# Kernel optimization log

Hardware: AMD Instinct MI355X
Metric: run time of the kernel (lower is better)

The kernel has to match this reference:

```python
import jax, jax.numpy as jnp
import numpy as np

B, H, D = 16, 16, 128          # batch (decode seqs), heads, head_dim
BLK = 16                        # paged-KV block size (hard-coded in source)
MAXB = 128                      # blocks per sequence
MAXS = MAXB * BLK               # 2048 max context
NBLK = B * MAXB                 # total cache blocks
SOFTMAX_SCALE = 1.0 / np.sqrt(D)


def setup_inputs() -> dict:
    key = jax.random.key(0)
    ks = jax.random.split(key, 8)
    Q = jax.random.normal(ks[0], (B, H, D), dtype=jnp.float32)
    K = jax.random.normal(ks[1], (B, H, D), dtype=jnp.float32)
    V = jax.random.normal(ks[2], (B, H, D), dtype=jnp.float32)
    Kcache = jax.random.normal(ks[3], (NBLK, BLK, H, D), dtype=jnp.float32)
    Vcache = jax.random.normal(ks[4], (NBLK, BLK, H, D), dtype=jnp.float32)
    # context length per sequence (includes the new decode token)
    input_length = jax.random.randint(ks[5], (B,), 1, MAXS + 1).astype(jnp.int32)
    # each sequence owns a contiguous run of blocks
    block_tables = jnp.arange(B * MAXB, dtype=jnp.int32).reshape(B, MAXB)
    # flat slot index where the new token's K/V are written
    pos = input_length - 1
    save_slots = (block_tables[jnp.arange(B), pos // BLK] * BLK + pos % BLK).astype(jnp.int64)
    # per-token RoPE cos/sin
    ang = jax.random.uniform(ks[6], (B, D), dtype=jnp.float32) * (2.0 * np.pi)
    cos, sin = jnp.cos(ang), jnp.sin(ang)
    mask = jnp.zeros((B, MAXS), dtype=jnp.float32)  # additive attention bias
    return {"Q": Q, "K": K, "V": V, "Kcache": Kcache, "Vcache": Vcache,
            "cos": cos, "sin": sin, "mask": mask,
            "input_length": input_length, "save_slots": save_slots,
            "block_tables": block_tables, "max_s": MAXS}


def _rope(x, cos, sin):
    # LLaMA rotate-half RoPE; cos/sin are [B,1,D], x is [B,H,D]
    d2 = x.shape[-1] // 2
    x1, x2 = x[..., :d2], x[..., d2:]
    rot = jnp.concatenate([-x2, x1], axis=-1)
    return x * cos + rot * sin


def reference(Q, K, V, Kcache, Vcache, cos, sin, mask,
              input_length, save_slots, block_tables, max_s):
    c = cos[:, None, :]
    s = sin[:, None, :]
    qr = _rope(Q, c, s)                      # [B,H,D]
    kr = _rope(K, c, s)                      # [B,H,D]
    # scatter new token K/V into the paged cache (flat slot view)
    Kf = Kcache.reshape(-1, H, D).at[save_slots].set(kr)
    Vf = Vcache.reshape(-1, H, D).at[save_slots].set(V)
    # gather each sequence's context slots via its block table
    slot_idx = (block_tables[:, :, None] * BLK
                + jnp.arange(BLK, dtype=jnp.int32)).reshape(B, MAXS)  # [B,S]
    keys = Kf[slot_idx]                      # [B,S,H,D]
    vals = Vf[slot_idx]                      # [B,S,H,D]
    scores = jnp.einsum('bhd,bshd->bhs', qr, keys) * SOFTMAX_SCALE + mask[:, None, :]
    valid = jnp.arange(MAXS, dtype=jnp.int32)[None, :] < input_length[:, None]
    scores = jnp.where(valid[:, None, :], scores, jnp.float32(-1e30))
    p = jax.nn.softmax(scores, axis=-1)
    out = jnp.einsum('bhs,bshd->bhd', p, vals)  # [B,H,D]
    return out
```

## Files before the change

kernel.cpp:

```cpp
#include <hip/hip_runtime.h>
#include <hip/hip_bf16.h>

#define BATCH 16
#define NHEAD 16
#define DHEAD 128
#define BLK   16
#define MAXB  128
#define MAXS  (MAXB * BLK)
#define NSPLIT 8
#define CHUNK  (MAXS / NSPLIT)
#define SCALE  0.0883883476483184f

#define WSQ_FLOATS (BATCH * NHEAD * DHEAD)
#define PART_STRIDE (DHEAD + 2)

__global__ void rope_scatter(const float* __restrict__ Q,
                             const float* __restrict__ K,
                             const float* __restrict__ V,
                             float* __restrict__ Kcache,
                             float* __restrict__ Vcache,
                             const float* __restrict__ cosb,
                             const float* __restrict__ sinb,
                             const int* __restrict__ save_slots,
                             float* __restrict__ ws_q) {
    const int bh = blockIdx.x;
    const int b  = bh / NHEAD;
    const int h  = bh % NHEAD;
    const int d  = threadIdx.x;

    const float c = cosb[b * DHEAD + d];
    const float s = sinb[b * DHEAD + d];

    const size_t qidx = (size_t)bh * DHEAD + d;
    const float qv = Q[qidx];
    const float qrot = (d < DHEAD / 2) ? -Q[qidx + DHEAD / 2] : Q[qidx - DHEAD / 2];
    ws_q[qidx] = qv * c + qrot * s;

    const float kv = K[qidx];
    const float krot = (d < DHEAD / 2) ? -K[qidx + DHEAD / 2] : K[qidx - DHEAD / 2];
    const float kr = kv * c + krot * s;

    const int slot = save_slots[b];
    const size_t cidx = (size_t)slot * (NHEAD * DHEAD) + (size_t)h * DHEAD + d;
    Kcache[cidx] = kr;
    Vcache[cidx] = V[qidx];
}

__global__ __launch_bounds__(256) void attn_partial(
        const float* __restrict__ Kcache,
        const float* __restrict__ Vcache,
        const float* __restrict__ mask,
        const int* __restrict__ input_length,
        const int* __restrict__ block_tables,
        const float* __restrict__ ws_q,
        float* __restrict__ ws_part) {
    const int split = blockIdx.x;
    const int h     = blockIdx.y;
    const int b     = blockIdx.z;
    const int tid   = threadIdx.x;
    const int wave  = tid >> 6;
    const int lane  = tid & 63;

    float* part = ws_part + ((size_t)((b * NHEAD + h) * NSPLIT + split)) * PART_STRIDE;

    const int L  = input_length[b];
    const int s0 = split * CHUNK;
    if (s0 >= L) {
        if (tid < DHEAD) part[tid] = 0.0f;
        if (tid == 0) { part[DHEAD] = -1e30f; part[DHEAD + 1] = 0.0f; }
        return;
    }
    const int n = min(CHUNK, L - s0);

    const float2 q = ((const float2*)(ws_q + (size_t)(b * NHEAD + h) * DHEAD))[lane];

    float m = -1e30f, l = 0.0f;
    float2 acc = make_float2(0.0f, 0.0f);

    for (int i = wave; i < n; i += 4) {
        const int s = s0 + i;
        const int slot = block_tables[b * MAXB + (s >> 4)] * BLK + (s & (BLK - 1));
        const size_t base = (size_t)slot * (NHEAD * DHEAD) + (size_t)h * DHEAD;
        const float2 k = ((const float2*)(Kcache + base))[lane];
        const float2 v = ((const float2*)(Vcache + base))[lane];

        float dot = k.x * q.x + k.y * q.y;
        #pragma unroll
        for (int off = 32; off >= 1; off >>= 1)
            dot += __shfl_xor(dot, off, 64);

        const float score = dot * SCALE + mask[(size_t)b * MAXS + s];
        const float mn    = fmaxf(m, score);
        const float p     = __expf(score - mn);
        const float alpha = __expf(m - mn);
        l = l * alpha + p;
        acc.x = acc.x * alpha + p * v.x;
        acc.y = acc.y * alpha + p * v.y;
        m = mn;
    }

    __shared__ float sm[4], sl[4];
    __shared__ float sacc[4][DHEAD];
    sacc[wave][2 * lane]     = acc.x;
    sacc[wave][2 * lane + 1] = acc.y;
    if (lane == 0) { sm[wave] = m; sl[wave] = l; }
    __syncthreads();

    if (tid < DHEAD) {
        float M = fmaxf(fmaxf(sm[0], sm[1]), fmaxf(sm[2], sm[3]));
        float a = 0.0f;
        #pragma unroll
        for (int w = 0; w < 4; ++w) a += sacc[w][tid] * __expf(sm[w] - M);
        part[tid] = a;
        if (tid == 0) {
            float lt = 0.0f;
            #pragma unroll
            for (int w = 0; w < 4; ++w) lt += sl[w] * __expf(sm[w] - M);
            part[DHEAD] = M;
            part[DHEAD + 1] = lt;
        }
    }
}

__global__ void attn_combine(const float* __restrict__ ws_part,
                             float* __restrict__ out) {
    const int bh = blockIdx.x;
    const int d  = threadIdx.x;

    const float* base = ws_part + (size_t)bh * NSPLIT * PART_STRIDE;

    float M = -1e30f;
    #pragma unroll
    for (int s = 0; s < NSPLIT; ++s)
        M = fmaxf(M, base[s * PART_STRIDE + DHEAD]);

    float lsum = 0.0f, a = 0.0f;
    #pragma unroll
    for (int s = 0; s < NSPLIT; ++s) {
        const float f = __expf(base[s * PART_STRIDE + DHEAD] - M);
        lsum += base[s * PART_STRIDE + DHEAD + 1] * f;
        a    += base[s * PART_STRIDE + d] * f;
    }
    out[(size_t)bh * DHEAD + d] = a / lsum;
}

extern "C" void kernel_launch(void* const* d_in, const int* in_sizes, int n_in,
                              void* d_out, int out_size, void* d_ws, size_t ws_size,
                              hipStream_t stream) {
    const float* Q       = (const float*)d_in[0];
    const float* K       = (const float*)d_in[1];
    const float* V       = (const float*)d_in[2];
    float*       Kcache  = (float*)d_in[3];
    float*       Vcache  = (float*)d_in[4];
    const float* cosb    = (const float*)d_in[5];
    const float* sinb    = (const float*)d_in[6];
    const float* mask    = (const float*)d_in[7];
    const int*   in_len  = (const int*)d_in[8];
    const int*   slots   = (const int*)d_in[9];
    const int*   btab    = (const int*)d_in[10];

    float* ws_q    = (float*)d_ws;
    float* ws_part = ws_q + WSQ_FLOATS;
    float* out     = (float*)d_out;

    rope_scatter<<<BATCH * NHEAD, DHEAD, 0, stream>>>(
        Q, K, V, Kcache, Vcache, cosb, sinb, slots, ws_q);

    dim3 grid2(NSPLIT, NHEAD, BATCH);
    attn_partial<<<grid2, 256, 0, stream>>>(
        Kcache, Vcache, mask, in_len, btab, ws_q, ws_part);

    attn_combine<<<BATCH * NHEAD, DHEAD, 0, stream>>>(ws_part, out);
}
```

Measured before the change: 515.2 us.

## Process tokens with half-wave float4 loads and two tokens per iteration

Each 32-lane half-wave now handles one token using float4 loads of K and V, giving 8 concurrent token streams per block instead of 4. The main loop unrolls by two tokens to issue more independent loads before the shuffle reduction and softmax update. The aim is more memory-level parallelism and fewer shuffle steps in this bandwidth-bound paged attention. The cost is more registers per thread and a larger cross-group merge in shared memory.

New measurement: 492.6 us. -4.4%, faster.

```diff
diff --git a/kernel.cpp b/kernel.cpp
--- a/kernel.cpp
+++ b/kernel.cpp
@@ -58,8 +58,8 @@
     const int h     = blockIdx.y;
     const int b     = blockIdx.z;
     const int tid   = threadIdx.x;
-    const int wave  = tid >> 6;
-    const int lane  = tid & 63;
+    const int hw    = tid >> 5;
+    const int ln    = tid & 31;
 
     float* part = ws_part + ((size_t)((b * NHEAD + h) * NSPLIT + split)) * PART_STRIDE;
 
@@ -72,50 +72,86 @@
     }
     const int n = min(CHUNK, L - s0);
 
-    const float2 q = ((const float2*)(ws_q + (size_t)(b * NHEAD + h) * DHEAD))[lane];
+    const float4 q = ((const float4*)(ws_q + (size_t)(b * NHEAD + h) * DHEAD))[ln];
+    const float* mrow = mask + (size_t)b * MAXS + s0;
+    const int*   bt   = block_tables + b * MAXB;
 
     float m = -1e30f, l = 0.0f;
-    float2 acc = make_float2(0.0f, 0.0f);
-
-    for (int i = wave; i < n; i += 4) {
+    float4 acc = make_float4(0.0f, 0.0f, 0.0f, 0.0f);
+
+    int i = hw;
+    for (; i + 8 < n; i += 16) {
+        const int sA = s0 + i;
+        const int sB = sA + 8;
+        const size_t baseA = (size_t)(bt[sA >> 4] * BLK + (sA & (BLK - 1))) * (NHEAD * DHEAD)
+                           + (size_t)h * DHEAD;
+        const size_t baseB = (size_t)(bt[sB >> 4] * BLK + (sB & (BLK - 1))) * (NHEAD * DHEAD)
+                           + (size_t)h * DHEAD;
+        const float4 kA = ((const float4*)(Kcache + baseA))[ln];
+        const float4 kB = ((const float4*)(Kcache + baseB))[ln];
+        const float4 vA = ((const float4*)(Vcache + baseA))[ln];
+        const float4 vB = ((const float4*)(Vcache + baseB))[ln];
+
+        float dA = kA.x * q.x + kA.y * q.y + kA.z * q.z + kA.w * q.w;
+        float dB = kB.x * q.x + kB.y * q.y + kB.z * q.z + kB.w * q.w;
+        #pragma unroll
+        for (int off = 16; off >= 1; off >>= 1) {
+            dA += __shfl_xor(dA, off, 64);
+            dB += __shfl_xor(dB, off, 64);
+        }
+
+        const float scA = dA * SCALE + mrow[i];
+        const float scB = dB * SCALE + mrow[i + 8];
+        const float mn  = fmaxf(m, fmaxf(scA, scB));
+        const float pA  = __expf(scA - mn);
+        const float pB  = __expf(scB - mn);
+        const float al  = __expf(m - mn);
+        l = l * al + pA + pB;
+        acc.x = acc.x * al + pA * vA.x + pB * vB.x;
+        acc.y = acc.y * al + pA * vA.y + pB * vB.y;
+        acc.z = acc.z * al + pA * vA.z + pB * vB.z;
+        acc.w = acc.w * al + pA * vA.w + pB * vB.w;
+        m = mn;
+    }
+    if (i < n) {
         const int s = s0 + i;
-        const int slot = block_tables[b * MAXB + (s >> 4)] * BLK + (s & (BLK - 1));
-        const size_t base = (size_t)slot * (NHEAD * DHEAD) + (size_t)h * DHEAD;
-        const float2 k = ((const float2*)(Kcache + base))[lane];
-        const float2 v = ((const float2*)(Vcache + base))[lane];
-
-        float dot = k.x * q.x + k.y * q.y;
-        #pragma unroll
-        for (int off = 32; off >= 1; off >>= 1)
-            dot += __shfl_xor(dot, off, 64);
-
-        const float score = dot * SCALE + mask[(size_t)b * MAXS + s];
-        const float mn    = fmaxf(m, score);
-        const float p     = __expf(score - mn);
-        const float alpha = __expf(m - mn);
-        l = l * alpha + p;
-        acc.x = acc.x * alpha + p * v.x;
-        acc.y = acc.y * alpha + p * v.y;
+        const size_t base = (size_t)(bt[s >> 4] * BLK + (s & (BLK - 1))) * (NHEAD * DHEAD)
+                          + (size_t)h * DHEAD;
+        const float4 k = ((const float4*)(Kcache + base))[ln];
+        const float4 v = ((const float4*)(Vcache + base))[ln];
+        float d = k.x * q.x + k.y * q.y + k.z * q.z + k.w * q.w;
+        #pragma unroll
+        for (int off = 16; off >= 1; off >>= 1) d += __shfl_xor(d, off, 64);
+        const float sc = d * SCALE + mrow[i];
+        const float mn = fmaxf(m, sc);
+        const float p  = __expf(sc - mn);
+        const float al = __expf(m - mn);
+        l = l * al + p;
+        acc.x = acc.x * al + p * v.x;
+        acc.y = acc.y * al + p * v.y;
+        acc.z = acc.z * al + p * v.z;
+        acc.w = acc.w * al + p * v.w;
         m = mn;
     }
 
-    __shared__ float sm[4], sl[4];
-    __shared__ float sacc[4][DHEAD];
-    sacc[wave][2 * lane]     = acc.x;
-    sacc[wave][2 * lane + 1] = acc.y;
-    if (lane == 0) { sm[wave] = m; sl[wave] = l; }
+    __shared__ float sm[8], sl[8];
+    __shared__ float sacc[8][DHEAD];
+    ((float4*)sacc[hw])[ln] = acc;
+    if (ln == 0) { sm[hw] = m; sl[hw] = l; }
     __syncthreads();
 
     if (tid < DHEAD) {
-        float M = fmaxf(fmaxf(sm[0], sm[1]), fmaxf(sm[2], sm[3]));
+        float M = -1e30f;
+        #pragma unroll
+        for (int w = 0; w < 8; ++w) M = fmaxf(M, sm[w]);
         float a = 0.0f;
         #pragma unroll
-        for (int w = 0; w < 4; ++w) a += sacc[w][tid] * __expf(sm[w] - M);
+        for (int w = 0; w < 8; ++w) a += sacc[w][tid] * __expf(sm[w] - M);
         part[tid] = a;
         if (tid == 0) {
             float lt = 0.0f;
             #pragma unroll
-            for (int w = 0; w < 4; ++w) lt += sl[w] * __expf(sm[w] - M);
+            for (int w = 0; w < 8; ++w) lt += sl[w] * __expf(sm[w] - M);
             part[DHEAD] = M;
             part[DHEAD + 1] = lt;
         }
```

## Replace online softmax with two-pass scores-then-PV using half-wave float4 loads

Applied to the files above, without the earlier changes.

The partial attention kernel now precomputes slot base offsets into shared memory, then computes all QK dot products with 32-lane half-waves using float4 loads. It stores the scores in shared memory, does an exact block-wide max and sum reduction, and then runs a separate PV pass. This removes the per-token online-softmax rescaling, the serial exp chain and the per-token block_table lookups, and it doubles the number of in-flight rows per block. In exchange it adds several __syncthreads and loads K and V in separate passes, so their loads no longer overlap.

New measurement: 472.3 us. 1.09x faster.

```diff
diff --git a/kernel.cpp b/kernel.cpp
--- a/kernel.cpp
+++ b/kernel.cpp
@@ -58,8 +58,13 @@
     const int h     = blockIdx.y;
     const int b     = blockIdx.z;
     const int tid   = threadIdx.x;
-    const int wave  = tid >> 6;
-    const int lane  = tid & 63;
+    const int hw    = tid >> 5;
+    const int ln    = tid & 31;
+
+    __shared__ int   sbase[CHUNK];
+    __shared__ float sp[CHUNK];
+    __shared__ float sred[8];
+    __shared__ float sacc[8][DHEAD];
 
     float* part = ws_part + ((size_t)((b * NHEAD + h) * NSPLIT + split)) * PART_STRIDE;
 
@@ -72,53 +77,63 @@
     }
     const int n = min(CHUNK, L - s0);
 
-    const float2 q = ((const float2*)(ws_q + (size_t)(b * NHEAD + h) * DHEAD))[lane];
+    if (tid < n) {
+        const int s = s0 + tid;
+        sbase[tid] = block_tables[b * MAXB + (s >> 4)] * (BLK * NHEAD * DHEAD)
+                   + (s & (BLK - 1)) * (NHEAD * DHEAD) + h * DHEAD;
+    }
+    const float4 q = ((const float4*)(ws_q + (size_t)(b * NHEAD + h) * DHEAD))[ln];
+    __syncthreads();
 
-    float m = -1e30f, l = 0.0f;
-    float2 acc = make_float2(0.0f, 0.0f);
+    #pragma unroll 4
+    for (int i = hw; i < n; i += 8) {
+        const float4 k = ((const float4*)(Kcache + sbase[i]))[ln];
+        float d = k.x * q.x + k.y * q.y + k.z * q.z + k.w * q.w;
+        #pragma unroll
+        for (int off = 16; off >= 1; off >>= 1)
+            d += __shfl_xor(d, off, 64);
+        if (ln == 0) sp[i] = d;
+    }
+    __syncthreads();
 
-    for (int i = wave; i < n; i += 4) {
-        const int s = s0 + i;
-        const int slot = block_tables[b * MAXB + (s >> 4)] * BLK + (s & (BLK - 1));
-        const size_t base = (size_t)slot * (NHEAD * DHEAD) + (size_t)h * DHEAD;
-        const float2 k = ((const float2*)(Kcache + base))[lane];
-        const float2 v = ((const float2*)(Vcache + base))[lane];
+    const float sc = (tid < n) ? sp[tid] * SCALE + mask[(size_t)b * MAXS + s0 + tid]
+                               : -1e30f;
+    float wm = sc;
+    #pragma unroll
+    for (int off = 32; off >= 1; off >>= 1)
+        wm = fmaxf(wm, __shfl_xor(wm, off, 64));
+    if ((tid & 63) == 0) sred[tid >> 6] = wm;
+    __syncthreads();
+    const float M = fmaxf(fmaxf(sred[0], sred[1]), fmaxf(sred[2], sred[3]));
+    const float p = (tid < n) ? __expf(sc - M) : 0.0f;
+    sp[tid] = p;
+    float wsum = p;
+    #pragma unroll
+    for (int off = 32; off >= 1; off >>= 1)
+        wsum += __shfl_xor(wsum, off, 64);
+    if ((tid & 63) == 0) sred[4 + (tid >> 6)] = wsum;
+    __syncthreads();
+    const float l = (sred[4] + sred[5]) + (sred[6] + sred[7]);
 
-        float dot = k.x * q.x + k.y * q.y;
-        #pragma unroll
-        for (int off = 32; off >= 1; off >>= 1)
-            dot += __shfl_xor(dot, off, 64);
-
-        const float score = dot * SCALE + mask[(size_t)b * MAXS + s];
-        const float mn    = fmaxf(m, score);
-        const float p     = __expf(score - mn);
-        const float alpha = __expf(m - mn);
-        l = l * alpha + p;
-        acc.x = acc.x * alpha + p * v.x;
-        acc.y = acc.y * alpha + p * v.y;
-        m = mn;
+    float4 acc = make_float4(0.0f, 0.0f, 0.0f, 0.0f);
+    #pragma unroll 4
+    for (int i = hw; i < n; i += 8) {
+        const float4 v = ((const float4*)(Vcache + sbase[i]))[ln];
+        const float pi = sp[i];
+        acc.x += pi * v.x;
+        acc.y += pi * v.y;
+        acc.z += pi * v.z;
+        acc.w += pi * v.w;
     }
 
-    __shared__ float sm[4], sl[4];
-    __shared__ float sacc[4][DHEAD];
-    sacc[wave][2 * lane]     = acc.x;
-    sacc[wave][2 * lane + 1] = acc.y;
-    if (lane == 0) { sm[wave] = m; sl[wave] = l; }
+    ((float4*)sacc[hw])[ln] = acc;
     __syncthreads();
-
     if (tid < DHEAD) {
-        float M = fmaxf(fmaxf(sm[0], sm[1]), fmaxf(sm[2], sm[3]));
         float a = 0.0f;
         #pragma unroll
-        for (int w = 0; w < 4; ++w) a += sacc[w][tid] * __expf(sm[w] - M);
+        for (int w = 0; w < 8; ++w) a += sacc[w][tid];
         part[tid] = a;
-        if (tid == 0) {
-            float lt = 0.0f;
-            #pragma unroll
-            for (int w = 0; w < 4; ++w) lt += sl[w] * __expf(sm[w] - M);
-            part[DHEAD] = M;
-            part[DHEAD + 1] = lt;
-        }
+        if (tid == 0) { part[DHEAD] = M; part[DHEAD + 1] = l; }
     }
 }
 
```
